# Performance work log

Hardware: AMD Instinct MI355X
Metric: run time of the kernel (lower is better)

Reference implementation:

```python
import jax, jax.numpy as jnp
import numpy as np

N, C, T, D, E, K = 50000, 32, 12, 128, 1600000, 3
LN_EPS = 1e-5


def setup_inputs() -> dict:
    key = jax.random.key(0)
    ks = jax.random.split(key, 6)
    x = jax.random.normal(ks[0], (N, C, T), dtype=jnp.float32)
    edge_index = jax.random.randint(ks[1], (2, E), 0, N, dtype=jnp.int32)
    Wx = jax.random.normal(ks[2], (4, K, C, D), dtype=jnp.float32) * 0.05
    bx = jnp.zeros((4, D), jnp.float32)
    Wh = jax.random.normal(ks[3], (4, K, D, D), dtype=jnp.float32) * 0.05
    bh = jnp.zeros((4, D), jnp.float32)
    wc = jax.random.normal(ks[4], (3, D), dtype=jnp.float32) * 0.05
    bg = jnp.zeros((4, D), jnp.float32)
    ln_gamma = jnp.ones((D,), jnp.float32)
    ln_beta = jnp.zeros((D,), jnp.float32)
    return dict(x=x, edge_index=edge_index, Wx=Wx, bx=bx, Wh=Wh, bh=bh,
                wc=wc, bg=bg, ln_gamma=ln_gamma, ln_beta=ln_beta)


def _edge_norm(edge_index, num_nodes):
    # PyG ChebConv sym normalization with lambda_max=2: L_hat = -D^{-1/2} A D^{-1/2}
    # (diagonal of L_hat is exactly 0 after the fill_value=-1 self-loop shift).
    src, dst = edge_index[0], edge_index[1]
    deg = jax.ops.segment_sum(jnp.ones(src.shape, jnp.float32), src, num_segments=num_nodes)
    dis = jnp.where(deg > 0, jax.lax.rsqrt(jnp.maximum(deg, 1e-12)), 0.0)
    w = -dis[src] * dis[dst]
    return src, dst, w


def reference(x, edge_index, Wx, bx, Wh, bh, wc, bg, ln_gamma, ln_beta):
    num_nodes = x.shape[0]
    src, dst, w = _edge_norm(edge_index, num_nodes)

    def lhat(v):  # [N, F] -> [N, F], sparse L_hat @ v via gather/scatter
        return jax.ops.segment_sum(w[:, None] * v[src], dst, num_segments=num_nodes)

    def cheb(v, W, b):  # Chebyshev conv, W: [K, F_in, F_out] (K >= 2 here)
        Tx0 = v
        out = Tx0 @ W[0]
        Tx1 = lhat(Tx0)
        out = out + Tx1 @ W[1]
        for k in range(2, W.shape[0]):
            Tx2 = 2.0 * lhat(Tx1) - Tx0
            out = out + Tx2 @ W[k]
            Tx0, Tx1 = Tx1, Tx2
        return out + b

    def step(carry, x_t):  # x_t: [N, C]
        h, c = carry
        gi = cheb(x_t, Wx[0], bx[0]) + cheb(h, Wh[0], bh[0])
        gf = cheb(x_t, Wx[1], bx[1]) + cheb(h, Wh[1], bh[1])
        gc = cheb(x_t, Wx[2], bx[2]) + cheb(h, Wh[2], bh[2])
        go = cheb(x_t, Wx[3], bx[3]) + cheb(h, Wh[3], bh[3])
        i = jax.nn.sigmoid(gi + wc[0] * c + bg[0])
        f = jax.nn.sigmoid(gf + wc[1] * c + bg[1])
        c_new = f * c + i * jnp.tanh(gc + bg[2])
        o = jax.nn.sigmoid(go + wc[2] * c_new + bg[3])
        h_new = o * jnp.tanh(c_new)
        # torch code appends h.detach() each step
        return (h_new, c_new), jax.lax.stop_gradient(h_new)

    h0 = jnp.zeros((num_nodes, Wh.shape[-1]), x.dtype)
    c0 = jnp.zeros_like(h0)
    xs = jnp.moveaxis(x, -1, 0)  # [T, N, C]
    _, H = jax.lax.scan(step, (h0, c0), xs)  # H: [T, N, D]

    H = jnp.tanh(H)  # activation='tanh'
    mu = jnp.mean(H, axis=-1, keepdims=True)
    var = jnp.var(H, axis=-1, keepdims=True)
    H = (H - mu) * jax.lax.rsqrt(var + LN_EPS) * ln_gamma + ln_beta  # LayerNorm(conv_dim)
    # Dropout is identity in eval mode; linear head is None.
    return H
```

## Files before the change

### kernel.cpp

```cpp
#include <hip/hip_runtime.h>
#include <math.h>

static constexpr int C_IN    = 32;
static constexpr int T_STEPS = 12;
static constexpr int D_HID   = 128;
static constexpr int KTOT    = 3*C_IN + 3*D_HID;
static constexpr int GDIM    = 4*D_HID;
static constexpr int XW      = T_STEPS*C_IN;
static constexpr int HW      = 3*D_HID;

static inline int cdiv(long a, int b) { return (int)((a + b - 1) / b); }

typedef __attribute__((ext_vector_type(8))) short bf16x8;
typedef __attribute__((ext_vector_type(4))) float f32x4;

__device__ __forceinline__ float bf2f(unsigned int u16) {
  union { unsigned int u; float f; } v; v.u = u16 << 16; return v.f;
}
__device__ __forceinline__ unsigned short f2bf(float f) {
  union { float f; unsigned int u; } v; v.f = f;
  unsigned int u = v.u + 0x7fffu + ((v.u >> 16) & 1u);
  return (unsigned short)(u >> 16);
}
__device__ __forceinline__ void split2(float a, unsigned short& h, unsigned short& l) {
  h = f2bf(a);
  l = f2bf(a - bf2f(h));
}
__device__ __forceinline__ float fsig(float x) { return 1.0f/(1.0f + __expf(-x)); }
__device__ __forceinline__ float ftanh(float x) {
  float e = __expf(2.0f*x);
  return 1.0f - 2.0f/(e + 1.0f);
}


__global__ void k_zero_i(int* __restrict__ p, int n) {
  int i = blockIdx.x*blockDim.x + threadIdx.x;
  if (i < n) p[i] = 0;
}

__global__ void k_count(const int* __restrict__ src, const int* __restrict__ dst,
                        int* __restrict__ cnt, int* __restrict__ deg, int E) {
  int e = blockIdx.x*blockDim.x + threadIdx.x;
  if (e < E) {
    atomicAdd(&cnt[dst[e]], 1);
    atomicAdd(&deg[src[e]], 1);
  }
}

__global__ void k_dis(const int* __restrict__ deg, float* __restrict__ dis, int n) {
  int i = blockIdx.x*blockDim.x + threadIdx.x;
  if (i < n) {
    int d = deg[i];
    dis[i] = d > 0 ? rsqrtf((float)d) : 0.0f;
  }
}

__global__ __launch_bounds__(1024) void k_scan(const int* __restrict__ cnt,
                                               int* __restrict__ rowptr, int n) {
  __shared__ int wsum[16];
  __shared__ int carry_s;
  int tid = threadIdx.x; int lane = tid & 63; int wv_ = tid >> 6;
  if (tid == 0) { carry_s = 0; rowptr[0] = 0; }
  __syncthreads();
  for (int base = 0; base < n; base += 1024) {
    int i = base + tid;
    int s = (i < n) ? cnt[i] : 0;
    #pragma unroll
    for (int off = 1; off < 64; off <<= 1) {
      int t = __shfl_up(s, off);
      if (lane >= off) s += t;
    }
    if (lane == 63) wsum[wv_] = s;
    __syncthreads();
    if (tid < 16) {
      int ws = wsum[tid];
      #pragma unroll
      for (int off = 1; off < 16; off <<= 1) {
        int t = __shfl_up(ws, off);
        if (tid >= off) ws += t;
      }
      wsum[tid] = ws;
    }
    __syncthreads();
    int offw = carry_s + (wv_ > 0 ? wsum[wv_-1] : 0);
    if (i < n) rowptr[i+1] = offw + s;
    __syncthreads();
    if (tid == 0) carry_s = carry_s + wsum[15];
    __syncthreads();
  }
}

__global__ void k_fill(const int* __restrict__ src, const int* __restrict__ dst,
                       const int* __restrict__ rowptr, int* __restrict__ fil,
                       const float* __restrict__ dis,
                       int* __restrict__ colI, float* __restrict__ wvv, int E) {
  int e = blockIdx.x*blockDim.x + threadIdx.x;
  if (e < E) {
    int d = dst[e], s = src[e];
    int p = rowptr[d] + atomicAdd(&fil[d], 1);
    colI[p] = s;
    wvv[p] = -dis[s] * dis[d];
  }
}


__global__ void k_packB(const float* __restrict__ Wx, const float* __restrict__ Wh,
                        unsigned short* __restrict__ BH, unsigned short* __restrict__ BL) {
  int idx = blockIdx.x*blockDim.x + threadIdx.x;
  if (idx >= KTOT*GDIM) return;
  int kk = idx / GDIM, p = idx % GDIM;
  int g = p & 3, d = p >> 2;
  float v;
  if (kk < 96) {
    int k3 = kk >> 5, c = kk & 31;
    auto wx = [&](int k) { return Wx[((((size_t)g*3 + k)*32 + c) << 7) + d]; };
    v = (k3 == 0) ? wx(0) - wx(2) : (k3 == 1) ? wx(1) : 2.0f*wx(2);
  } else {
    int kk2 = kk - 96;
    int k3 = kk2 >> 7, j = kk2 & 127;
    auto wh = [&](int k) { return Wh[((((size_t)g*3 + k)*128 + j) << 7) + d]; };
    v = (k3 == 0) ? wh(0) - wh(2) : (k3 == 1) ? wh(1) : 2.0f*wh(2);
  }
  unsigned short h, l; split2(v, h, l);
  int kt = kk >> 5, kg = (kk >> 3) & 3, i = kk & 7;
  size_t o = ((size_t)((kt*4 + kg)*GDIM + p))*8 + i;
  BH[o] = h; BL[o] = l;
}

__global__ void k_bias(const float* __restrict__ bx, const float* __restrict__ bh,
                       const float* __restrict__ bg, float* __restrict__ bsum) {
  int i = blockIdx.x*blockDim.x + threadIdx.x;
  if (i < GDIM) bsum[i] = bx[i] + bh[i] + bg[i];
}


__global__ void k_xt_all(const float* __restrict__ x, unsigned short* __restrict__ P0,
                         long total) {
  long i = (long)blockIdx.x*blockDim.x + threadIdx.x;
  if (i >= total) return;
  int c = (int)(i & 31);
  long nt = i >> 5;
  int t = (int)(nt % T_STEPS);
  long n = nt / T_STEPS;
  float v = x[(n*C_IN + c)*T_STEPS + t];
  P0[n*XW + t*C_IN + c] = f2bf(v);
}

__global__ void k_spmm_x(const int* __restrict__ rowptr, const int* __restrict__ colI,
                         const float* __restrict__ wvv,
                         const unsigned short* __restrict__ SRC,
                         unsigned short* __restrict__ DST, int n) {
  int gt = blockIdx.x*blockDim.x + threadIdx.x;
  int node = gt / 96;
  int lane = gt - node*96;
  if (node >= n) return;
  const uint2* gp = (const uint2*)SRC;
  float a0 = 0.f, a1 = 0.f, a2 = 0.f, a3 = 0.f;
  int r0 = rowptr[node], r1 = rowptr[node+1];
  int e = r0;
  for (; e + 4 <= r1; e += 4) {
    int s0 = colI[e], s1 = colI[e+1], s2 = colI[e+2], s3 = colI[e+3];
    float w0 = wvv[e], w1 = wvv[e+1], w2 = wvv[e+2], w3 = wvv[e+3];
    uint2 u0 = gp[(size_t)s0*96 + lane];
    uint2 u1 = gp[(size_t)s1*96 + lane];
    uint2 u2 = gp[(size_t)s2*96 + lane];
    uint2 u3 = gp[(size_t)s3*96 + lane];
    a0 += w0*bf2f(u0.x & 0xffffu) + w1*bf2f(u1.x & 0xffffu)
        + w2*bf2f(u2.x & 0xffffu) + w3*bf2f(u3.x & 0xffffu);
    a1 += w0*bf2f(u0.x >> 16)     + w1*bf2f(u1.x >> 16)
        + w2*bf2f(u2.x >> 16)     + w3*bf2f(u3.x >> 16);
    a2 += w0*bf2f(u0.y & 0xffffu) + w1*bf2f(u1.y & 0xffffu)
        + w2*bf2f(u2.y & 0xffffu) + w3*bf2f(u3.y & 0xffffu);
    a3 += w0*bf2f(u0.y >> 16)     + w1*bf2f(u1.y >> 16)
        + w2*bf2f(u2.y >> 16)     + w3*bf2f(u3.y >> 16);
  }
  for (; e < r1; ++e) {
    int s = colI[e]; float w = wvv[e];
    uint2 u = gp[(size_t)s*96 + lane];
    a0 += w*bf2f(u.x & 0xffffu);
    a1 += w*bf2f(u.x >> 16);
    a2 += w*bf2f(u.y & 0xffffu);
    a3 += w*bf2f(u.y >> 16);
  }
  uint2 hw;
  hw.x = (unsigned int)f2bf(a0) | ((unsigned int)f2bf(a1) << 16);
  hw.y = (unsigned int)f2bf(a2) | ((unsigned int)f2bf(a3) << 16);
  ((uint2*)DST)[(size_t)node*96 + lane] = hw;
}

__global__ void k_spmm_h(const int* __restrict__ rowptr, const int* __restrict__ colI,
                         const float* __restrict__ wvv,
                         const unsigned short* __restrict__ GSRC,
                         unsigned short* __restrict__ HB,
                         unsigned short* __restrict__ GOUT, int colO, int selfCol, int n) {
  int gt = blockIdx.x*blockDim.x + threadIdx.x;
  int node = gt >> 5;
  int lane = gt & 31;
  if (node >= n) return;
  const uint2* gp = (const uint2*)GSRC;
  if (selfCol >= 0) {
    uint2 own = gp[(size_t)node*32 + lane];
    ((uint2*)HB)[(((size_t)node*HW + selfCol) >> 2) + lane] = own;
  }
  float a0 = 0.f, a1 = 0.f, a2 = 0.f, a3 = 0.f;
  int r0 = rowptr[node], r1 = rowptr[node+1];
  int e = r0;
  for (; e + 4 <= r1; e += 4) {
    int s0 = colI[e], s1 = colI[e+1], s2 = colI[e+2], s3 = colI[e+3];
    float w0 = wvv[e], w1 = wvv[e+1], w2 = wvv[e+2], w3 = wvv[e+3];
    uint2 u0 = gp[(size_t)s0*32 + lane];
    uint2 u1 = gp[(size_t)s1*32 + lane];
    uint2 u2 = gp[(size_t)s2*32 + lane];
    uint2 u3 = gp[(size_t)s3*32 + lane];
    a0 += w0*bf2f(u0.x & 0xffffu) + w1*bf2f(u1.x & 0xffffu)
        + w2*bf2f(u2.x & 0xffffu) + w3*bf2f(u3.x & 0xffffu);
    a1 += w0*bf2f(u0.x >> 16)     + w1*bf2f(u1.x >> 16)
        + w2*bf2f(u2.x >> 16)     + w3*bf2f(u3.x >> 16);
    a2 += w0*bf2f(u0.y & 0xffffu) + w1*bf2f(u1.y & 0xffffu)
        + w2*bf2f(u2.y & 0xffffu) + w3*bf2f(u3.y & 0xffffu);
    a3 += w0*bf2f(u0.y >> 16)     + w1*bf2f(u1.y >> 16)
        + w2*bf2f(u2.y >> 16)     + w3*bf2f(u3.y >> 16);
  }
  for (; e < r1; ++e) {
    int s = colI[e]; float w = wvv[e];
    uint2 u = gp[(size_t)s*32 + lane];
    a0 += w*bf2f(u.x & 0xffffu);
    a1 += w*bf2f(u.x >> 16);
    a2 += w*bf2f(u.y & 0xffffu);
    a3 += w*bf2f(u.y >> 16);
  }
  uint2 hw;
  hw.x = (unsigned int)f2bf(a0) | ((unsigned int)f2bf(a1) << 16);
  hw.y = (unsigned int)f2bf(a2) | ((unsigned int)f2bf(a3) << 16);
  ((uint2*)HB)[(((size_t)node*HW + colO) >> 2) + lane] = hw;
  if (GOUT) ((uint2*)GOUT)[(size_t)node*32 + lane] = hw;
}


__global__ __launch_bounds__(256) void k_gemm_lstm(
    const unsigned short* __restrict__ P0, const unsigned short* __restrict__ P1,
    const unsigned short* __restrict__ P2, const unsigned short* __restrict__ HB,
    const unsigned short* __restrict__ BH, const unsigned short* __restrict__ BL,
    const float* __restrict__ bsum, const float* __restrict__ wcp,
    float* __restrict__ Cst, float* __restrict__ Ht,
    unsigned short* __restrict__ HG,
    int N, int first, int ntk, int t) {
  union SMem {
    struct { unsigned short As[128][42]; unsigned short Bs[2][4][1026]; } g;
    float ep[32][132];
  };
  __shared__ SMem sm;
  const int tid = threadIdx.x;
  int orig = blockIdx.y * gridDim.x + blockIdx.x;
  int nwg = gridDim.x * gridDim.y;
  int q8 = nwg >> 3, r8 = nwg & 7;
  int xcd = orig & 7, idx = orig >> 3;
  int newid = (xcd < r8 ? xcd*(q8+1) : r8*(q8+1) + (xcd-r8)*q8) + idx;
  const int bm = (newid >> 2) * 128;
  const int bxi = newid & 3;
  const int bn = bxi * 128;
  const int bx32 = bxi * 32;
  const int lane = tid & 63;
  const int wid = tid >> 6;
  const int wr = wid >> 1;
  const int wcol = wid & 1;
  const int l15 = lane & 15;
  const int l4  = lane >> 4;
  const int tcol = t*32;
  f32x4 acc[4][4] = {};
  for (int kt = 0; kt < ntk; ++kt) {
    const unsigned short* Asrc; int coff;
    if (kt == 0)      { Asrc = P0; coff = tcol; }
    else if (kt == 1) { Asrc = P1; coff = tcol; }
    else if (kt == 2) { Asrc = P2; coff = tcol; }
    else              { Asrc = HB; coff = (kt-3)*32; }
    __syncthreads();
    #pragma unroll
    for (int r2 = 0; r2 < 2; ++r2) {
      int cc = tid + 256*r2;
      int row = cc >> 2, ko = (cc & 3) * 8;
      uint4 vh = make_uint4(0,0,0,0);
      if (bm + row < N) vh = *(const uint4*)(Asrc + (size_t)(bm + row)*384 + coff + ko);
      *(uint4*)&sm.g.As[row][ko] = vh;
      int kg = cc >> 7, col = cc & 127;
      size_t bo = ((size_t)((kt*4 + kg)*GDIM + bn + col))*8;
      *(uint4*)&sm.g.Bs[0][kg][col*8] = *(const uint4*)(BH + bo);
      *(uint4*)&sm.g.Bs[1][kg][col*8] = *(const uint4*)(BL + bo);
    }
    __syncthreads();
    bf16x8 ah[4];
    #pragma unroll
    for (int mi = 0; mi < 4; ++mi) {
      int r = wr*64 + mi*16 + l15;
      ah[mi] = *(const bf16x8*)&sm.g.As[r][l4*8];
    }
    #pragma unroll
    for (int ni = 0; ni < 4; ++ni) {
      int cidx = (wcol*64 + ni*16 + l15)*8;
      bf16x8 bh8 = *(const bf16x8*)&sm.g.Bs[0][l4][cidx];
      bf16x8 bl8 = *(const bf16x8*)&sm.g.Bs[1][l4][cidx];
      #pragma unroll
      for (int mi = 0; mi < 4; ++mi) {
        acc[mi][ni] = __builtin_amdgcn_mfma_f32_16x16x32_bf16(ah[mi], bh8, acc[mi][ni], 0,0,0);
        acc[mi][ni] = __builtin_amdgcn_mfma_f32_16x16x32_bf16(ah[mi], bl8, acc[mi][ni], 0,0,0);
      }
    }
  }
  for (int mi = 0; mi < 4; ++mi) {
    __syncthreads();
    #pragma unroll
    for (int ni = 0; ni < 4; ++ni)
      #pragma unroll
      for (int q = 0; q < 4; ++q)
        sm.ep[wr*16 + l4*4 + q][wcol*64 + ni*16 + l15] = acc[mi][ni][q];
    __syncthreads();
    #pragma unroll
    for (int r = 0; r < 4; ++r) {
      int item = tid + 256*r;
      int rloc = item >> 5, dd = item & 31;
      int row = bm + (rloc >> 4)*64 + mi*16 + (rloc & 15);
      if (row >= N) continue;
      int dg = bx32 + dd;
      f32x4 gv = *(f32x4*)&sm.ep[rloc][dd*4];
      float c0 = first ? 0.0f : Cst[(size_t)row*D_HID + dg];
      float gi = gv[0] + bsum[dg]       + wcp[dg]*c0;
      float gf = gv[1] + bsum[128+dg]   + wcp[128+dg]*c0;
      float gc = gv[2] + bsum[256+dg];
      float go = gv[3] + bsum[384+dg];
      float ig = fsig(gi), fg = fsig(gf);
      float cn = fg*c0 + ig*ftanh(gc);
      float og = fsig(go + wcp[256+dg]*cn);
      float hn = og*ftanh(cn);
      Cst[(size_t)row*D_HID + dg] = cn;
      Ht[(size_t)row*D_HID + dg] = hn;
      HG[(size_t)row*D_HID + dg] = f2bf(hn);
    }
  }
}


__global__ __launch_bounds__(256) void k_ln(float* __restrict__ H, const float* __restrict__ gam,
                                            const float* __restrict__ bet, long rows) {
  long row = (long)blockIdx.x*4 + (threadIdx.x >> 6);
  int lane = threadIdx.x & 63;
  if (row >= rows) return;
  float* p = H + row*(long)D_HID;
  float a = ftanh(p[lane]);
  float b = ftanh(p[lane+64]);
  float s = a + b, q = a*a + b*b;
  #pragma unroll
  for (int off = 32; off > 0; off >>= 1) {
    s += __shfl_xor(s, off);
    q += __shfl_xor(q, off);
  }
  float mu  = s * (1.0f/128.0f);
  float var = q * (1.0f/128.0f) - mu*mu;
  float rs  = rsqrtf(var + 1e-5f);
  p[lane]    = (a - mu)*rs*gam[lane]    + bet[lane];
  p[lane+64] = (b - mu)*rs*gam[lane+64] + bet[lane+64];
}


extern "C" void kernel_launch(void* const* d_in, const int* in_sizes, int n_in,
                              void* d_out, int out_size, void* d_ws, size_t ws_size,
                              hipStream_t stream) {
  const float* x   = (const float*)d_in[0];
  const int*   ei  = (const int*)  d_in[1];
  const float* Wx  = (const float*)d_in[2];
  const float* bx  = (const float*)d_in[3];
  const float* Wh  = (const float*)d_in[4];
  const float* bh  = (const float*)d_in[5];
  const float* wc  = (const float*)d_in[6];
  const float* bg  = (const float*)d_in[7];
  const float* lng = (const float*)d_in[8];
  const float* lnb = (const float*)d_in[9];
  const int N = in_sizes[0] / (C_IN*T_STEPS);
  const int E = in_sizes[1] / 2;
  const int* src = ei;
  const int* dst = ei + E;
  float* Hout = (float*)d_out;

  char* w = (char*)d_ws;
  auto alloc = [&](size_t bytes) -> char* {
    char* p = w; w += (bytes + 255) & ~size_t(255); return p;
  };
  unsigned short* P0 = (unsigned short*)alloc((size_t)N*XW*2);
  unsigned short* P1 = (unsigned short*)alloc((size_t)N*XW*2);
  unsigned short* P2 = (unsigned short*)alloc((size_t)N*XW*2);
  unsigned short* HB = (unsigned short*)alloc((size_t)N*HW*2);
  float* Cst   = (float*)alloc((size_t)N*D_HID*4);
  int*   aux   = (int*)  alloc((size_t)3*N*4);
  float* dis   = (float*)alloc((size_t)N*4);
  int*   rowptr= (int*)  alloc((size_t)(N+1)*4);
  int*   colI  = (int*)  alloc((size_t)E*4);
  float* wvv   = (float*)alloc((size_t)E*4);
  unsigned short* BH = (unsigned short*)alloc((size_t)KTOT*GDIM*2);
  unsigned short* BL = (unsigned short*)alloc((size_t)KTOT*GDIM*2);
  float* bsum  = (float*)alloc((size_t)GDIM*4);
  unsigned short* HG   = (unsigned short*)alloc((size_t)N*D_HID*2);
  unsigned short* Y1HG = (unsigned short*)alloc((size_t)N*D_HID*2);
  if ((size_t)(w - (char*)d_ws) > ws_size) return;

  int* cnt = aux; int* fil = aux + N; int* deg = aux + 2*N;

  k_zero_i<<<cdiv(3L*N,256),256,0,stream>>>(aux, 3*N);
  k_count<<<cdiv(E,256),256,0,stream>>>(src, dst, cnt, deg, E);
  k_dis<<<cdiv(N,256),256,0,stream>>>(deg, dis, N);
  k_scan<<<1,1024,0,stream>>>(cnt, rowptr, N);
  k_fill<<<cdiv(E,256),256,0,stream>>>(src, dst, rowptr, fil, dis, colI, wvv, E);
  k_packB<<<cdiv((long)KTOT*GDIM,256),256,0,stream>>>(Wx, Wh, BH, BL);
  k_bias<<<2,256,0,stream>>>(bx, bh, bg, bsum);

  k_xt_all<<<cdiv((long)N*XW,256),256,0,stream>>>(x, P0, (long)N*XW);
  k_spmm_x<<<cdiv((long)N*96,256),256,0,stream>>>(rowptr, colI, wvv, P0, P1, N);
  k_spmm_x<<<cdiv((long)N*96,256),256,0,stream>>>(rowptr, colI, wvv, P1, P2, N);

  dim3 ggrid(GDIM/128, cdiv(N,128));
  for (int t = 0; t < T_STEPS; ++t) {
    if (t > 0) {
      k_spmm_h<<<cdiv((long)N*32,256),256,0,stream>>>(rowptr, colI, wvv,
          HG, HB, Y1HG, 128, 0, N);
      k_spmm_h<<<cdiv((long)N*32,256),256,0,stream>>>(rowptr, colI, wvv,
          Y1HG, HB, nullptr, 256, -1, N);
    }
    int ntk = (t == 0) ? 3 : KTOT/32;
    k_gemm_lstm<<<ggrid,256,0,stream>>>(P0, P1, P2, HB, BH, BL, bsum, wc,
        Cst, Hout + (size_t)t*N*D_HID, HG, N, t == 0 ? 1 : 0, ntk, t);
  }
  k_ln<<<cdiv((long)T_STEPS*N,4),256,0,stream>>>(Hout, lng, lnb, (long)T_STEPS*N);
}
```

Before: 3.221 ms.

## Widen SpMM lanes to 16-byte loads and register-prefetch GEMM tiles

The hidden-state SpMM now uses 16 threads per node, each loading 16 bytes (8 bf16) per neighbor instead of 8 bytes, with a 2-way edge unroll. This halves the threads per gather and widens memory transactions. The fused GEMM-LSTM kernel now prefetches the next K-tile's A/B data into registers while computing on the current shared-memory tile, hiding global-load latency. The cost is higher register pressure in the GEMM and fewer threads in flight per node in the SpMM.

```diff
diff --git a/kernel.cpp b/kernel.cpp
--- a/kernel.cpp
+++ b/kernel.cpp
@@ -194,46 +194,52 @@
                          unsigned short* __restrict__ HB,
                          unsigned short* __restrict__ GOUT, int colO, int selfCol, int n) {
   int gt = blockIdx.x*blockDim.x + threadIdx.x;
-  int node = gt >> 5;
-  int lane = gt & 31;
+  int node = gt >> 4;
+  int lane = gt & 15;
   if (node >= n) return;
-  const uint2* gp = (const uint2*)GSRC;
+  const char* gb = (const char*)GSRC + (lane << 4);
   if (selfCol >= 0) {
-    uint2 own = gp[(size_t)node*32 + lane];
-    ((uint2*)HB)[(((size_t)node*HW + selfCol) >> 2) + lane] = own;
-  }
-  float a0 = 0.f, a1 = 0.f, a2 = 0.f, a3 = 0.f;
+    uint4 own = *(const uint4*)(gb + ((unsigned)node << 8));
+    *(uint4*)((char*)(HB + (size_t)node*HW + selfCol) + (lane << 4)) = own;
+  }
+  float a0=0.f,a1=0.f,a2=0.f,a3=0.f,a4=0.f,a5=0.f,a6=0.f,a7=0.f;
   int r0 = rowptr[node], r1 = rowptr[node+1];
   int e = r0;
-  for (; e + 4 <= r1; e += 4) {
-    int s0 = colI[e], s1 = colI[e+1], s2 = colI[e+2], s3 = colI[e+3];
-    float w0 = wvv[e], w1 = wvv[e+1], w2 = wvv[e+2], w3 = wvv[e+3];
-    uint2 u0 = gp[(size_t)s0*32 + lane];
-    uint2 u1 = gp[(size_t)s1*32 + lane];
-    uint2 u2 = gp[(size_t)s2*32 + lane];
-    uint2 u3 = gp[(size_t)s3*32 + lane];
-    a0 += w0*bf2f(u0.x & 0xffffu) + w1*bf2f(u1.x & 0xffffu)
-        + w2*bf2f(u2.x & 0xffffu) + w3*bf2f(u3.x & 0xffffu);
-    a1 += w0*bf2f(u0.x >> 16)     + w1*bf2f(u1.x >> 16)
-        + w2*bf2f(u2.x >> 16)     + w3*bf2f(u3.x >> 16);
-    a2 += w0*bf2f(u0.y & 0xffffu) + w1*bf2f(u1.y & 0xffffu)
-        + w2*bf2f(u2.y & 0xffffu) + w3*bf2f(u3.y & 0xffffu);
-    a3 += w0*bf2f(u0.y >> 16)     + w1*bf2f(u1.y >> 16)
-        + w2*bf2f(u2.y >> 16)     + w3*bf2f(u3.y >> 16);
-  }
-  for (; e < r1; ++e) {
-    int s = colI[e]; float w = wvv[e];
-    uint2 u = gp[(size_t)s*32 + lane];
-    a0 += w*bf2f(u.x & 0xffffu);
-    a1 += w*bf2f(u.x >> 16);
-    a2 += w*bf2f(u.y & 0xffffu);
-    a3 += w*bf2f(u.y >> 16);
-  }
-  uint2 hw;
+  for (; e + 2 <= r1; e += 2) {
+    unsigned o0 = (unsigned)colI[e]   << 8;
+    unsigned o1 = (unsigned)colI[e+1] << 8;
+    float w0 = wvv[e], w1 = wvv[e+1];
+    uint4 u0 = *(const uint4*)(gb + o0);
+    uint4 u1 = *(const uint4*)(gb + o1);
+    a0 += w0*bf2f(u0.x & 0xffffu) + w1*bf2f(u1.x & 0xffffu);
+    a1 += w0*bf2f(u0.x >> 16)     + w1*bf2f(u1.x >> 16);
+    a2 += w0*bf2f(u0.y & 0xffffu) + w1*bf2f(u1.y & 0xffffu);
+    a3 += w0*bf2f(u0.y >> 16)     + w1*bf2f(u1.y >> 16);
+    a4 += w0*bf2f(u0.z & 0xffffu) + w1*bf2f(u1.z & 0xffffu);
+    a5 += w0*bf2f(u0.z >> 16)     + w1*bf2f(u1.z >> 16);
+    a6 += w0*bf2f(u0.w & 0xffffu) + w1*bf2f(u1.w & 0xffffu);
+    a7 += w0*bf2f(u0.w >> 16)     + w1*bf2f(u1.w >> 16);
+  }
+  if (e < r1) {
+    unsigned o0 = (unsigned)colI[e] << 8;
+    float w0 = wvv[e];
+    uint4 u0 = *(const uint4*)(gb + o0);
+    a0 += w0*bf2f(u0.x & 0xffffu);
+    a1 += w0*bf2f(u0.x >> 16);
+    a2 += w0*bf2f(u0.y & 0xffffu);
+    a3 += w0*bf2f(u0.y >> 16);
+    a4 += w0*bf2f(u0.z & 0xffffu);
+    a5 += w0*bf2f(u0.z >> 16);
+    a6 += w0*bf2f(u0.w & 0xffffu);
+    a7 += w0*bf2f(u0.w >> 16);
+  }
+  uint4 hw;
   hw.x = (unsigned int)f2bf(a0) | ((unsigned int)f2bf(a1) << 16);
   hw.y = (unsigned int)f2bf(a2) | ((unsigned int)f2bf(a3) << 16);
-  ((uint2*)HB)[(((size_t)node*HW + colO) >> 2) + lane] = hw;
-  if (GOUT) ((uint2*)GOUT)[(size_t)node*32 + lane] = hw;
+  hw.z = (unsigned int)f2bf(a4) | ((unsigned int)f2bf(a5) << 16);
+  hw.w = (unsigned int)f2bf(a6) | ((unsigned int)f2bf(a7) << 16);
+  *(uint4*)((char*)(HB + (size_t)node*HW + colO) + (lane << 4)) = hw;
+  if (GOUT) ((uint4*)GOUT)[((size_t)node << 4) + lane] = hw;
 }
 
 
@@ -267,27 +273,46 @@
   const int l15 = lane & 15;
   const int l4  = lane >> 4;
   const int tcol = t*32;
-  f32x4 acc[4][4] = {};
-  for (int kt = 0; kt < ntk; ++kt) {
+
+  uint4 ra[2], rbh[2], rbl[2];
+  auto issue = [&](int kt) {
     const unsigned short* Asrc; int coff;
     if (kt == 0)      { Asrc = P0; coff = tcol; }
     else if (kt == 1) { Asrc = P1; coff = tcol; }
     else if (kt == 2) { Asrc = P2; coff = tcol; }
     else              { Asrc = HB; coff = (kt-3)*32; }
-    __syncthreads();
     #pragma unroll
     for (int r2 = 0; r2 < 2; ++r2) {
       int cc = tid + 256*r2;
       int row = cc >> 2, ko = (cc & 3) * 8;
       uint4 vh = make_uint4(0,0,0,0);
       if (bm + row < N) vh = *(const uint4*)(Asrc + (size_t)(bm + row)*384 + coff + ko);
-      *(uint4*)&sm.g.As[row][ko] = vh;
+      ra[r2] = vh;
       int kg = cc >> 7, col = cc & 127;
       size_t bo = ((size_t)((kt*4 + kg)*GDIM + bn + col))*8;
-      *(uint4*)&sm.g.Bs[0][kg][col*8] = *(const uint4*)(BH + bo);
-      *(uint4*)&sm.g.Bs[1][kg][col*8] = *(const uint4*)(BL + bo);
-    }
-    __syncthreads();
+      rbh[r2] = *(const uint4*)(BH + bo);
+      rbl[r2] = *(const uint4*)(BL + bo);
+    }
+  };
+  auto commit = [&]() {
+    #pragma unroll
+    for (int r2 = 0; r2 < 2; ++r2) {
+      int cc = tid + 256*r2;
+      int row = cc >> 2, ko = (cc & 3) * 8;
+      *(uint4*)&sm.g.As[row][ko] = ra[r2];
+      int kg = cc >> 7, col = cc & 127;
+      *(uint4*)&sm.g.Bs[0][kg][col*8] = rbh[r2];
+      *(uint4*)&sm.g.Bs[1][kg][col*8] = rbl[r2];
+    }
+  };
+
+  f32x4 acc[4][4] = {};
+  issue(0);
+  for (int kt = 0; kt < ntk; ++kt) {
+    __syncthreads();
+    commit();
+    __syncthreads();
+    if (kt + 1 < ntk) issue(kt + 1);
     bf16x8 ah[4];
     #pragma unroll
     for (int mi = 0; mi < 4; ++mi) {
@@ -418,9 +443,9 @@
   dim3 ggrid(GDIM/128, cdiv(N,128));
   for (int t = 0; t < T_STEPS; ++t) {
     if (t > 0) {
-      k_spmm_h<<<cdiv((long)N*32,256),256,0,stream>>>(rowptr, colI, wvv,
+      k_spmm_h<<<cdiv((long)N*16,256),256,0,stream>>>(rowptr, colI, wvv,
           HG, HB, Y1HG, 128, 0, N);
-      k_spmm_h<<<cdiv((long)N*32,256),256,0,stream>>>(rowptr, colI, wvv,
+      k_spmm_h<<<cdiv((long)N*16,256),256,0,stream>>>(rowptr, colI, wvv,
           Y1HG, HB, nullptr, 256, -1, N);
     }
     int ntk = (t == 0) ? 3 : KTOT/32;
```

Result: slower. 3.923 ms (+21.8%).

## Restructure hidden-state SpMM into column chunks with edge-parallel lanes and vector loads

Applied to the files above, without the earlier changes.

Rewrites the per-step SpMM over the hidden state. Each node is now handled by 16 threads: 4 column slices of 16 bytes each, times 4 edge phases, with a 4-column-chunk grid dimension. Partial sums are reduced with shuffles, and the 128-bit gathers are meant to raise memory-level parallelism and cut per-edge instruction overhead. The LayerNorm kernel is also changed to use float4 loads, with 32 lanes per row. The chunked grid re-reads rowptr and colI once per column chunk, which adds index traffic.

```diff
diff --git a/kernel.cpp b/kernel.cpp
--- a/kernel.cpp
+++ b/kernel.cpp
@@ -193,47 +193,50 @@
                          const unsigned short* __restrict__ GSRC,
                          unsigned short* __restrict__ HB,
                          unsigned short* __restrict__ GOUT, int colO, int selfCol, int n) {
-  int gt = blockIdx.x*blockDim.x + threadIdx.x;
-  int node = gt >> 5;
-  int lane = gt & 31;
+  const int chunk = blockIdx.x;
+  const int t16 = threadIdx.x & 15;
+  const int slice = t16 & 3;
+  const int ephase = t16 >> 2;
+  const int node = blockIdx.y*16 + (threadIdx.x >> 4);
   if (node >= n) return;
-  const uint2* gp = (const uint2*)GSRC;
-  if (selfCol >= 0) {
-    uint2 own = gp[(size_t)node*32 + lane];
-    ((uint2*)HB)[(((size_t)node*HW + selfCol) >> 2) + lane] = own;
-  }
-  float a0 = 0.f, a1 = 0.f, a2 = 0.f, a3 = 0.f;
+  const unsigned sub = ((unsigned)chunk << 6) + ((unsigned)slice << 4);
+  const char* gb = (const char*)GSRC + sub;
+  float a0=0.f,a1=0.f,a2=0.f,a3=0.f,a4=0.f,a5=0.f,a6=0.f,a7=0.f;
   int r0 = rowptr[node], r1 = rowptr[node+1];
-  int e = r0;
-  for (; e + 4 <= r1; e += 4) {
-    int s0 = colI[e], s1 = colI[e+1], s2 = colI[e+2], s3 = colI[e+3];
-    float w0 = wvv[e], w1 = wvv[e+1], w2 = wvv[e+2], w3 = wvv[e+3];
-    uint2 u0 = gp[(size_t)s0*32 + lane];
-    uint2 u1 = gp[(size_t)s1*32 + lane];
-    uint2 u2 = gp[(size_t)s2*32 + lane];
-    uint2 u3 = gp[(size_t)s3*32 + lane];
-    a0 += w0*bf2f(u0.x & 0xffffu) + w1*bf2f(u1.x & 0xffffu)
-        + w2*bf2f(u2.x & 0xffffu) + w3*bf2f(u3.x & 0xffffu);
-    a1 += w0*bf2f(u0.x >> 16)     + w1*bf2f(u1.x >> 16)
-        + w2*bf2f(u2.x >> 16)     + w3*bf2f(u3.x >> 16);
-    a2 += w0*bf2f(u0.y & 0xffffu) + w1*bf2f(u1.y & 0xffffu)
-        + w2*bf2f(u2.y & 0xffffu) + w3*bf2f(u3.y & 0xffffu);
-    a3 += w0*bf2f(u0.y >> 16)     + w1*bf2f(u1.y >> 16)
-        + w2*bf2f(u2.y >> 16)     + w3*bf2f(u3.y >> 16);
-  }
-  for (; e < r1; ++e) {
-    int s = colI[e]; float w = wvv[e];
-    uint2 u = gp[(size_t)s*32 + lane];
+  for (int e = r0 + ephase; e < r1; e += 4) {
+    unsigned off = (unsigned)colI[e] << 8;
+    float w = wvv[e];
+    uint4 u = *(const uint4*)(gb + off);
     a0 += w*bf2f(u.x & 0xffffu);
     a1 += w*bf2f(u.x >> 16);
     a2 += w*bf2f(u.y & 0xffffu);
     a3 += w*bf2f(u.y >> 16);
-  }
-  uint2 hw;
-  hw.x = (unsigned int)f2bf(a0) | ((unsigned int)f2bf(a1) << 16);
-  hw.y = (unsigned int)f2bf(a2) | ((unsigned int)f2bf(a3) << 16);
-  ((uint2*)HB)[(((size_t)node*HW + colO) >> 2) + lane] = hw;
-  if (GOUT) ((uint2*)GOUT)[(size_t)node*32 + lane] = hw;
+    a4 += w*bf2f(u.z & 0xffffu);
+    a5 += w*bf2f(u.z >> 16);
+    a6 += w*bf2f(u.w & 0xffffu);
+    a7 += w*bf2f(u.w >> 16);
+  }
+  a0 += __shfl_xor(a0, 4); a1 += __shfl_xor(a1, 4);
+  a2 += __shfl_xor(a2, 4); a3 += __shfl_xor(a3, 4);
+  a4 += __shfl_xor(a4, 4); a5 += __shfl_xor(a5, 4);
+  a6 += __shfl_xor(a6, 4); a7 += __shfl_xor(a7, 4);
+  a0 += __shfl_xor(a0, 8); a1 += __shfl_xor(a1, 8);
+  a2 += __shfl_xor(a2, 8); a3 += __shfl_xor(a3, 8);
+  a4 += __shfl_xor(a4, 8); a5 += __shfl_xor(a5, 8);
+  a6 += __shfl_xor(a6, 8); a7 += __shfl_xor(a7, 8);
+  if (ephase == 0) {
+    uint4 hw;
+    hw.x = (unsigned int)f2bf(a0) | ((unsigned int)f2bf(a1) << 16);
+    hw.y = (unsigned int)f2bf(a2) | ((unsigned int)f2bf(a3) << 16);
+    hw.z = (unsigned int)f2bf(a4) | ((unsigned int)f2bf(a5) << 16);
+    hw.w = (unsigned int)f2bf(a6) | ((unsigned int)f2bf(a7) << 16);
+    *(uint4*)((char*)(HB + (size_t)node*HW + colO) + sub) = hw;
+    if (GOUT) *(uint4*)((char*)(GOUT + (size_t)node*D_HID) + sub) = hw;
+    if (selfCol >= 0) {
+      uint4 own = *(const uint4*)(gb + ((unsigned)node << 8));
+      *(uint4*)((char*)(HB + (size_t)node*HW + selfCol) + sub) = own;
+    }
+  }
 }
 
 
@@ -341,23 +344,30 @@
 
 __global__ __launch_bounds__(256) void k_ln(float* __restrict__ H, const float* __restrict__ gam,
                                             const float* __restrict__ bet, long rows) {
-  long row = (long)blockIdx.x*4 + (threadIdx.x >> 6);
-  int lane = threadIdx.x & 63;
+  long row = (long)blockIdx.x*8 + (threadIdx.x >> 5);
+  int l32 = threadIdx.x & 31;
   if (row >= rows) return;
-  float* p = H + row*(long)D_HID;
-  float a = ftanh(p[lane]);
-  float b = ftanh(p[lane+64]);
-  float s = a + b, q = a*a + b*b;
+  float* p = H + row*(long)D_HID + l32*4;
+  float4 v = *(float4*)p;
+  float b0 = ftanh(v.x), b1 = ftanh(v.y), b2 = ftanh(v.z), b3 = ftanh(v.w);
+  float s = b0 + b1 + b2 + b3;
+  float q = b0*b0 + b1*b1 + b2*b2 + b3*b3;
   #pragma unroll
-  for (int off = 32; off > 0; off >>= 1) {
+  for (int off = 16; off > 0; off >>= 1) {
     s += __shfl_xor(s, off);
     q += __shfl_xor(q, off);
   }
   float mu  = s * (1.0f/128.0f);
   float var = q * (1.0f/128.0f) - mu*mu;
   float rs  = rsqrtf(var + 1e-5f);
-  p[lane]    = (a - mu)*rs*gam[lane]    + bet[lane];
-  p[lane+64] = (b - mu)*rs*gam[lane+64] + bet[lane+64];
+  float4 g = *(const float4*)(gam + l32*4);
+  float4 be = *(const float4*)(bet + l32*4);
+  float4 o;
+  o.x = (b0 - mu)*rs*g.x + be.x;
+  o.y = (b1 - mu)*rs*g.y + be.y;
+  o.z = (b2 - mu)*rs*g.z + be.z;
+  o.w = (b3 - mu)*rs*g.w + be.w;
+  *(float4*)p = o;
 }
 
 
@@ -416,16 +426,17 @@
   k_spmm_x<<<cdiv((long)N*96,256),256,0,stream>>>(rowptr, colI, wvv, P1, P2, N);
 
   dim3 ggrid(GDIM/128, cdiv(N,128));
+  dim3 sgrid(4, cdiv(N,16));
   for (int t = 0; t < T_STEPS; ++t) {
     if (t > 0) {
-      k_spmm_h<<<cdiv((long)N*32,256),256,0,stream>>>(rowptr, colI, wvv,
+      k_spmm_h<<<sgrid,256,0,stream>>>(rowptr, colI, wvv,
           HG, HB, Y1HG, 128, 0, N);
-      k_spmm_h<<<cdiv((long)N*32,256),256,0,stream>>>(rowptr, colI, wvv,
+      k_spmm_h<<<sgrid,256,0,stream>>>(rowptr, colI, wvv,
           Y1HG, HB, nullptr, 256, -1, N);
     }
     int ntk = (t == 0) ? 3 : KTOT/32;
     k_gemm_lstm<<<ggrid,256,0,stream>>>(P0, P1, P2, HB, BH, BL, bsum, wc,
         Cst, Hout + (size_t)t*N*D_HID, HG, N, t == 0 ? 1 : 0, ntk, t);
   }
-  k_ln<<<cdiv((long)T_STEPS*N,4),256,0,stream>>>(Hout, lng, lnb, (long)T_STEPS*N);
-}
+  k_ln<<<cdiv((long)T_STEPS*N,8),256,0,stream>>>(Hout, lng, lnb, (long)T_STEPS*N);
+}
```

Result: slower. 3.842 ms (+19.3%).
